# Kernel tuning notes

Hardware: AMD Instinct MI355X
Metric: run time of the kernel (lower is better)

Reference implementation:

```python
import jax, jax.numpy as jnp
import numpy as np

HID = 2048
NH = 16
NKV = 16
HD = HID // NH          # 128
ROPE_BASE = 100000.0
ROPE_SCALE = 4.0
B, L = 2, 2048
NEG = -1e9


def rope(x, offset=0):
    # x: [B, NH, L, HD]; half-split (rotate-half) RoPE with linear scaling
    Lx = x.shape[2]
    D = HD // 2
    pos = (jnp.arange(offset, offset + Lx, dtype=jnp.float32) / ROPE_SCALE)  # [L]
    freq = jnp.exp(-jnp.arange(D, dtype=jnp.float32) * (np.log(ROPE_BASE) / D))  # [D]
    m_theta = pos[:, None] * freq[None, :]          # [L, D]
    cos, sin = jnp.cos(m_theta), jnp.sin(m_theta)
    x1, x2 = x[..., :D], x[..., D:]
    rx1 = x1 * cos - x2 * sin
    rx2 = x1 * sin + x2 * cos
    return jnp.concatenate([rx1, rx2], axis=-1)


def setup_inputs() -> dict:
    key = jax.random.key(0)
    ks = jax.random.split(key, 5)
    x = jax.random.normal(ks[0], (B, L, HID), dtype=jnp.float32)
    # additive causal mask [1,1,L,L]
    mask = jnp.triu(jnp.full((L, L), NEG, dtype=jnp.float32), k=1)[None, None]
    Wq = jax.random.normal(ks[1], (HID, NH * HD), dtype=jnp.float32) * 0.02
    Wk = jax.random.normal(ks[2], (HID, NKV * HD), dtype=jnp.float32) * 0.02
    Wv = jax.random.normal(ks[3], (HID, NKV * HD), dtype=jnp.float32) * 0.02
    Wo = jax.random.normal(ks[4], (NH * HD, HID), dtype=jnp.float32) * 0.02
    return {"x": x, "mask": mask, "Wq": Wq, "Wk": Wk, "Wv": Wv, "Wo": Wo}


def reference(x, mask, Wq, Wk, Wv, Wo):
    b, l, _ = x.shape
    scale = HD ** -0.5
    q = (x @ Wq).reshape(b, l, NH, HD).transpose(0, 2, 1, 3)    # [B,NH,L,HD]
    k = (x @ Wk).reshape(b, l, NKV, HD).transpose(0, 2, 1, 3)
    v = (x @ Wv).reshape(b, l, NKV, HD).transpose(0, 2, 1, 3)
    rep = NH // NKV
    if rep > 1:
        k = jnp.repeat(k, rep, axis=1)
        v = jnp.repeat(v, rep, axis=1)
    q = rope(q)
    k = rope(k)
    scores = scale * jnp.einsum('bhqd,bhkd->bhqk', q, k)        # [B,NH,L,L]
    scores = scores + mask
    attn = jax.nn.softmax(scores, axis=-1)
    out = jnp.einsum('bhqk,bhkd->bhqd', attn, v)                # [B,NH,L,HD]
    out = out.transpose(0, 2, 1, 3).reshape(b, l, NH * HD)
    return out @ Wo
```

## Files before the change

### kernel.cpp

```cpp
#include <hip/hip_runtime.h>
#include <math.h>

#define BB   2
#define LL   2048
#define HIDD 2048
#define NHH  16
#define HDD  128
#define QKVN 6144
#define THR2 11.5416f

typedef unsigned short u16;
typedef float  f32x4 __attribute__((ext_vector_type(4)));
typedef __bf16 bf16x8 __attribute__((ext_vector_type(8)));

static __device__ __forceinline__ float exp2_fast(float x){
  return __builtin_amdgcn_exp2f(x);
}
static __device__ __forceinline__ u16 f2bf(float x){
  unsigned u = __float_as_uint(x);
  return (u16)((u + 0x7fffu + ((u >> 16) & 1u)) >> 16);
}
static __device__ __forceinline__ float bf2f(u16 b){
  return __uint_as_float(((unsigned)b) << 16);
}
static __device__ __forceinline__ void gl_lds16(const void* g, void* l){
  __builtin_amdgcn_global_load_lds(
      (__attribute__((address_space(1))) void*)(void*)g,
      (__attribute__((address_space(3))) void*)l,
      16, 0, 0);
}


__global__ void cvt_f32_bf16_k(const float* __restrict__ src, u16* __restrict__ dst, int n4){
  int i = blockIdx.x * blockDim.x + threadIdx.x;
  if (i >= n4) return;
  float4 v = ((const float4*)src)[i];
  ushort4 o;
  o.x = f2bf(v.x); o.y = f2bf(v.y); o.z = f2bf(v.z); o.w = f2bf(v.w);
  ((ushort4*)dst)[i] = o;
}

__global__ void transpose_cvt_k(const float* __restrict__ src, u16* __restrict__ dst, int R, int C){
  __shared__ float t[32][33];
  int c0 = blockIdx.x * 32, r0 = blockIdx.y * 32;
  int tx = threadIdx.x, ty = threadIdx.y;
  #pragma unroll
  for (int i = 0; i < 32; i += 8) t[ty + i][tx] = src[(size_t)(r0 + ty + i) * C + c0 + tx];
  __syncthreads();
  #pragma unroll
  for (int i = 0; i < 32; i += 8) dst[(size_t)(c0 + ty + i) * R + r0 + tx] = f2bf(t[tx][ty + i]);
}

__global__ void rope_k(u16* __restrict__ qkv){
  int idx = blockIdx.x * blockDim.x + threadIdx.x;
  int d   = idx & 63;
  int h   = (idx >> 6) & 15;
  int row = idx >> 10;
  int l   = row & (LL - 1);
  float fr = __expf(-(float)d * 0.17988946f);
  float th = (float)l * 0.25f * fr;
  float s, c;
  sincosf(th, &s, &c);
  size_t base = (size_t)row * QKVN + h * HDD + d;
  #pragma unroll
  for (int part = 0; part < 2; part++){
    float f = (part == 0) ? 0.12753375f : 1.0f;
    float x1 = bf2f(qkv[base]), x2 = bf2f(qkv[base + 64]);
    qkv[base]      = f2bf((x1 * c - x2 * s) * f);
    qkv[base + 64] = f2bf((x1 * s + x2 * c) * f);
    base += HIDD;
  }
}

__global__ void build_vt_k(const u16* __restrict__ qkv, u16* __restrict__ vt){
  __shared__ u16 t[32][33];
  int bh = blockIdx.z;
  int b = bh >> 4, h = bh & 15;
  const u16* src = qkv + (size_t)b * LL * QKVN + 2 * HIDD + h * HDD;
  u16* dst = vt + (size_t)bh * HDD * LL;
  int d0 = blockIdx.x * 32, l0 = blockIdx.y * 32;
  int tx = threadIdx.x, ty = threadIdx.y;
  #pragma unroll
  for (int i = 0; i < 32; i += 8) t[ty + i][tx] = src[(size_t)(l0 + ty + i) * QKVN + d0 + tx];
  __syncthreads();
  #pragma unroll
  for (int i = 0; i < 32; i += 8) dst[(size_t)(d0 + ty + i) * LL + l0 + tx] = t[tx][ty + i];
}


#define G2_STAGE(kt, bsel) do {                                                           \
  _Pragma("unroll")                                                                       \
  for (int i_ = 0; i_ < 2; i_++){                            \
    int c_ = ((i_ * 8 + wv) * 64) + lane;                                                 \
    int p_ = c_ * 16;                                                                     \
    int r_ = p_ >> 7; int cb_ = (p_ & 127) ^ ((r_ & 7) << 4);                             \
    gl_lds16(A + (size_t)(m0 + r_) * K + (kt) + (cb_ >> 1),                               \
             &AB[bsel][((i_ * 8 + wv) * 64) * 8]);                                        \
  }                                                                                       \
  _Pragma("unroll")                                                                       \
  for (int i_ = 0; i_ < 4; i_++){                            \
    int c_ = ((i_ * 8 + wv) * 64) + lane;                                                 \
    int p_ = c_ * 16;                                                                     \
    int r_ = p_ >> 7; int cb_ = (p_ & 127) ^ ((r_ & 7) << 4);                             \
    gl_lds16(Bt + (size_t)(n0 + r_) * K + (kt) + (cb_ >> 1),                              \
             &AB[bsel][8192 + ((i_ * 8 + wv) * 64) * 8]);                                 \
  }                                                                                       \
} while(0)

template<int OUT_BF16>
__global__ __launch_bounds__(512, 1) void gemm_bt2_k(
    const u16* __restrict__ A, const u16* __restrict__ Bt,
    void* __restrict__ Cout, int M, int N, int K)
{
  __shared__ __align__(16) u16 AB[2][24576];
  const int tid = threadIdx.x, lane = tid & 63, wv = tid >> 6;
  const int wr = wv >> 2, wc = wv & 3;
  const int m0 = blockIdx.y * 128, n0 = blockIdx.x * 256;
  const int rq = lane >> 4, cl = lane & 15;
  const int NT = K >> 6;

  const f32x4 Z = {0.f, 0.f, 0.f, 0.f};
  f32x4 acc[4][4];
  #pragma unroll
  for (int m = 0; m < 4; m++)
    #pragma unroll
    for (int n = 0; n < 4; n++) acc[m][n] = Z;

  G2_STAGE(0, 0);
  G2_STAGE(64, 1);
  asm volatile("s_waitcnt vmcnt(6)");
  __builtin_amdgcn_sched_barrier(0);
  __builtin_amdgcn_s_barrier();

  int cur = 0;
  for (int t = 0; t < NT; t++){
    const char* As_ = (const char*)&AB[cur][0];
    const char* Bs_ = (const char*)&AB[cur][8192];

    #pragma unroll
    for (int ks = 0; ks < 2; ks++){
      const int kb = ks * 64 + rq * 16;
      bf16x8 a[4], b[4];
      #pragma unroll
      for (int m = 0; m < 4; m++){
        int r = wr * 64 + m * 16 + cl;
        a[m] = *(const bf16x8*)(As_ + r * 128 + (kb ^ ((r & 7) << 4)));
      }
      #pragma unroll
      for (int n = 0; n < 4; n++){
        int r = wc * 64 + n * 16 + cl;
        b[n] = *(const bf16x8*)(Bs_ + r * 128 + (kb ^ ((r & 7) << 4)));
      }
      __builtin_amdgcn_s_setprio(1);
      #pragma unroll
      for (int m = 0; m < 4; m++)
        #pragma unroll
        for (int n = 0; n < 4; n++)
          acc[m][n] = __builtin_amdgcn_mfma_f32_16x16x32_bf16(a[m], b[n], acc[m][n], 0, 0, 0);
      __builtin_amdgcn_s_setprio(0);
    }

    __builtin_amdgcn_sched_barrier(0);
    __builtin_amdgcn_s_barrier();

    if (t + 2 < NT){
      G2_STAGE((t + 2) * 64, cur);
      asm volatile("s_waitcnt vmcnt(6)");
    } else {
      asm volatile("s_waitcnt vmcnt(0)");
    }
    __builtin_amdgcn_sched_barrier(0);
    __builtin_amdgcn_s_barrier();
    cur ^= 1;
  }

  #pragma unroll
  for (int m = 0; m < 4; m++){
    int gr0 = m0 + wr * 64 + m * 16 + rq * 4;
    #pragma unroll
    for (int n = 0; n < 4; n++){
      int gc = n0 + wc * 64 + n * 16 + cl;
      #pragma unroll
      for (int rr = 0; rr < 4; rr++){
        if (OUT_BF16) ((u16*)Cout)[(size_t)(gr0 + rr) * N + gc] = f2bf(acc[m][n][rr]);
        else          ((float*)Cout)[(size_t)(gr0 + rr) * N + gc] = acc[m][n][rr];
      }
    }
  }
}


#define STAGE_K(jj, bsel) do {                                                            \
  _Pragma("unroll")                                                                       \
  for (int i_ = 0; i_ < 2; i_++){                                                         \
    int fb_ = (i_ * 8 + wv) * 64;                                                         \
    int p_  = (fb_ + lane) * 16;                                                          \
    int r_ = p_ >> 8; int cb_ = (p_ & 255) ^ ((r_ & 7) << 4);                             \
    gl_lds16(qkv + (size_t)(b * LL + (jj) * 64 + r_) * QKVN + HIDD + h * HDD + (cb_ >> 1),\
             &Kb[bsel][fb_ * 8]);                                                         \
  }                                                                                       \
} while(0)

#define STAGE_V(jj) do {                                                                  \
  _Pragma("unroll")                                                                       \
  for (int i_ = 0; i_ < 2; i_++){                                                         \
    int fb_ = (i_ * 8 + wv) * 64;                                                         \
    int p_  = (fb_ + lane) * 16;                                                          \
    int r_ = p_ >> 7; int cb_ = (p_ & 127) ^ ((r_ & 7) << 4);                             \
    gl_lds16(vt + (size_t)(bh * HDD + r_) * LL + (jj) * 64 + (cb_ >> 1), &Vs[fb_ * 8]);   \
  }                                                                                       \
} while(0)

__global__ __launch_bounds__(512, 1) void attn_k(
    const u16* __restrict__ qkv, const u16* __restrict__ vt,
    u16* __restrict__ aout)
{
  __shared__ __align__(16) u16 Kb[2][64 * 128];
  __shared__ __align__(16) u16 Vs[128 * 64];
  const int tid = threadIdx.x, lane = tid & 63, wv = tid >> 6;
  const int bh = blockIdx.x;
  const int pr = blockIdx.y;
  const int b = bh >> 4, h = bh & 15;
  const int rq = lane >> 4, cl = lane & 15;

  bf16x8 ones;
  #pragma unroll
  for (int i = 0; i < 8; i++) ones[i] = (__bf16)1.0f;
  const f32x4 Z = {0.f, 0.f, 0.f, 0.f};

  int cur = 0;
  STAGE_K(0, 0);

  #pragma unroll
  for (int ph = 0; ph < 2; ph++){
    const int qt = ph ? pr : (15 - pr);
    const int nj = 2 * qt + 2;

    bf16x8 qf[4];
    {
      const u16* qb = qkv + (size_t)(b * LL + qt * 128 + wv * 16 + cl) * QKVN + h * HDD + rq * 8;
      #pragma unroll
      for (int ks = 0; ks < 4; ks++) qf[ks] = *(const bf16x8*)(qb + ks * 32);
    }

    f32x4 acco[8], accl;
    float mst[4];
    #pragma unroll
    for (int n = 0; n < 8; n++) acco[n] = Z;
    accl = Z;
    #pragma unroll
    for (int rr = 0; rr < 4; rr++) mst[rr] = -INFINITY;

    const int wrow_hi = qt * 128 + wv * 16 + 15;

    if (ph == 0) __syncthreads();

    for (int j = 0; j < nj; j++){
      if (j + 1 < nj)      STAGE_K(j + 1, cur ^ 1);
      else if (ph == 0)    STAGE_K(0,     cur ^ 1);
      STAGE_V(j);
      const bool act = (j * 64 <= wrow_hi);

      f32x4 sv[4];
      if (act){
        const char* KsC = (const char*)&Kb[cur][0];
        #pragma unroll
        for (int ct = 0; ct < 4; ct++) sv[ct] = Z;
        #pragma unroll
        for (int ks = 0; ks < 4; ks++){
          const int kb = ks * 64 + rq * 16;
          #pragma unroll
          for (int ct = 0; ct < 4; ct++){
            int r = ct * 16 + cl;
            bf16x8 bfr = *(const bf16x8*)(KsC + r * 256 + (kb ^ ((r & 7) << 4)));
            sv[ct] = __builtin_amdgcn_mfma_f32_16x16x32_bf16(qf[ks], bfr, sv[ct], 0, 0, 0);
          }
        }
      }

      __syncthreads();

      if (act){
        char* pbase = (char*)&Kb[cur][0] + wv * 2048;
        const bool msk = (j >= 2 * qt);

        float p4[4][4], lmx[4];
        #pragma unroll
        for (int rr = 0; rr < 4; rr++) lmx[rr] = -1e30f;
        const int qg = qt * 128 + wv * 16 + rq * 4;
        #pragma unroll
        for (int ct = 0; ct < 4; ct++){
          int col = j * 64 + ct * 16 + cl;
          #pragma unroll
          for (int rr = 0; rr < 4; rr++){
            float v = sv[ct][rr];
            if (msk && col > qg + rr) v = -1e30f;
            p4[ct][rr] = v;
            lmx[rr] = fmaxf(lmx[rr], v);
          }
        }
        float need = -1e30f;
        #pragma unroll
        for (int rr = 0; rr < 4; rr++) need = fmaxf(need, lmx[rr] - mst[rr]);
        if (__any(need > THR2)){
          float mx[4];
          #pragma unroll
          for (int rr = 0; rr < 4; rr++) mx[rr] = lmx[rr];
          #pragma unroll
          for (int off = 1; off < 16; off <<= 1)
            #pragma unroll
            for (int rr = 0; rr < 4; rr++)
              mx[rr] = fmaxf(mx[rr], __shfl_xor(mx[rr], off, 64));
          #pragma unroll
          for (int rr = 0; rr < 4; rr++){
            float mn  = fmaxf(mst[rr], mx[rr]);
            float fsc = exp2_fast(mst[rr] - mn);
            mst[rr] = mn;
            accl[rr] *= fsc;
            #pragma unroll
            for (int n = 0; n < 8; n++) acco[n][rr] *= fsc;
          }
        }
        #pragma unroll
        for (int ct = 0; ct < 4; ct++)
          #pragma unroll
          for (int rr = 0; rr < 4; rr++){
            float e = exp2_fast(p4[ct][rr] - mst[rr]);
            int wr = rq * 4 + rr;
            *(u16*)(pbase + wr * 128 + (((ct * 16 + cl) * 2) ^ ((wr & 7) << 4))) = f2bf(e);
          }

        const char* VsC = (const char*)Vs;
        #pragma unroll
        for (int ks = 0; ks < 2; ks++){
          const int kvb = ks * 64 + rq * 16;
          bf16x8 pa = *(const bf16x8*)(pbase + cl * 128 + (kvb ^ ((cl & 7) << 4)));
          accl = __builtin_amdgcn_mfma_f32_16x16x32_bf16(pa, ones, accl, 0, 0, 0);
          #pragma unroll
          for (int n = 0; n < 8; n++){
            int r = n * 16 + cl;
            bf16x8 bfr = *(const bf16x8*)(VsC + r * 128 + (kvb ^ ((r & 7) << 4)));
            acco[n] = __builtin_amdgcn_mfma_f32_16x16x32_bf16(pa, bfr, acco[n], 0, 0, 0);
          }
        }
      }

      __syncthreads();
      cur ^= 1;
    }

    #pragma unroll
    for (int rr = 0; rr < 4; rr++){
      float inv = 1.0f / accl[rr];
      size_t grow = (size_t)(b * LL + qt * 128 + wv * 16 + rq * 4 + rr);
      #pragma unroll
      for (int n = 0; n < 8; n++)
        aout[grow * HIDD + h * HDD + n * 16 + cl] = f2bf(acco[n][rr] * inv);
    }
  }
}


extern "C" void kernel_launch(void* const* d_in, const int* in_sizes, int n_in,
                              void* d_out, int out_size, void* d_ws, size_t ws_size,
                              hipStream_t stream)
{
  const float* x  = (const float*)d_in[0];
  const float* Wq = (const float*)d_in[2];
  const float* Wk = (const float*)d_in[3];
  const float* Wv = (const float*)d_in[4];
  const float* Wo = (const float*)d_in[5];
  float* out = (float*)d_out;

  if (ws_size < 134217728ull) return;

  char* ws = (char*)d_ws;
  u16* xb   = (u16*)(ws);
  u16* Wt   = (u16*)(ws + 16777216ull);
  u16* Wot  = (u16*)(ws + 41943040ull);
  u16* qkv  = (u16*)(ws + 50331648ull);
  u16* vt   = (u16*)(ws + 100663296ull);
  u16* aout = (u16*)(ws + 117440512ull);

  cvt_f32_bf16_k<<<2097152 / 256, 256, 0, stream>>>(x, xb, 2097152);
  dim3 tb(32, 8);
  transpose_cvt_k<<<dim3(64, 64), tb, 0, stream>>>(Wq, Wt,                   2048, 2048);
  transpose_cvt_k<<<dim3(64, 64), tb, 0, stream>>>(Wk, Wt + 2048 * 2048,     2048, 2048);
  transpose_cvt_k<<<dim3(64, 64), tb, 0, stream>>>(Wv, Wt + 2 * 2048 * 2048, 2048, 2048);
  transpose_cvt_k<<<dim3(64, 64), tb, 0, stream>>>(Wo, Wot,                  2048, 2048);

  gemm_bt2_k<1><<<dim3(6144 / 256, 4096 / 128), 512, 0, stream>>>(xb, Wt, qkv, 4096, 6144, 2048);
  rope_k<<<4194304 / 256, 256, 0, stream>>>(qkv);
  build_vt_k<<<dim3(4, 64, 32), tb, 0, stream>>>(qkv, vt);

  attn_k<<<dim3(32, 8), 512, 0, stream>>>(qkv, vt, aout);

  gemm_bt2_k<0><<<dim3(2048 / 256, 4096 / 128), 512, 0, stream>>>(aout, Wot, out, 4096, 2048, 2048);
}
```

Measured before the change: 279.2 us.

## Triple-buffer GEMM LDS and interleave global prefetch with four MFMA sub-phases

The bf16 GEMM moves from double to triple LDS buffering, so the load for tile t+2 can be issued while tile t is being computed, with no separate barrier-then-load step. Each K-tile is split into four phases of LDS reads plus MFMA, and the A and B global-to-LDS prefetches are spread across those phases with barriers between them. The goal is to overlap global loads with MFMA work and shorten the pipeline stall at the end of each iteration. The cost is 50% more LDS, more barriers per tile, and smaller register fragments per phase, and the changed vmcnt accounting risks mistakes.

```diff
diff --git a/kernel.cpp b/kernel.cpp
--- a/kernel.cpp
+++ b/kernel.cpp
@@ -88,23 +88,25 @@
 }
 
 
-#define G2_STAGE(kt, bsel) do {                                                           \
-  _Pragma("unroll")                                                                       \
-  for (int i_ = 0; i_ < 2; i_++){                            \
-    int c_ = ((i_ * 8 + wv) * 64) + lane;                                                 \
-    int p_ = c_ * 16;                                                                     \
-    int r_ = p_ >> 7; int cb_ = (p_ & 127) ^ ((r_ & 7) << 4);                             \
-    gl_lds16(A + (size_t)(m0 + r_) * K + (kt) + (cb_ >> 1),                               \
-             &AB[bsel][((i_ * 8 + wv) * 64) * 8]);                                        \
-  }                                                                                       \
-  _Pragma("unroll")                                                                       \
-  for (int i_ = 0; i_ < 4; i_++){                            \
-    int c_ = ((i_ * 8 + wv) * 64) + lane;                                                 \
-    int p_ = c_ * 16;                                                                     \
-    int r_ = p_ >> 7; int cb_ = (p_ & 127) ^ ((r_ & 7) << 4);                             \
-    gl_lds16(Bt + (size_t)(n0 + r_) * K + (kt) + (cb_ >> 1),                              \
-             &AB[bsel][8192 + ((i_ * 8 + wv) * 64) * 8]);                                 \
-  }                                                                                       \
+#define G2_STG_A(kt, bsel) do {                                                            \
+  _Pragma("unroll")                                                                        \
+  for (int i_ = 0; i_ < 2; i_++){                                                          \
+    int ci_ = ((i_ * 8 + wv) * 64) + lane;                                                 \
+    int p_ = ci_ * 16; int r_ = p_ >> 7; int cb_ = (p_ & 127) ^ ((r_ & 7) << 4);           \
+    gl_lds16(A + (size_t)(m0 + r_) * K + (kt) + (cb_ >> 1),                                \
+             &AB[bsel][((i_ * 8 + wv) * 64) * 8]);                                         \
+  }                                                                                        \
+} while(0)
+
+#define G2_STG_B(kt, bsel, hh) do {                                                        \
+  _Pragma("unroll")                                                                        \
+  for (int i_ = 0; i_ < 2; i_++){                                                          \
+    int bi_ = (hh) * 2 + i_;                                                               \
+    int ci_ = ((bi_ * 8 + wv) * 64) + lane;                                                \
+    int p_ = ci_ * 16; int r_ = p_ >> 7; int cb_ = (p_ & 127) ^ ((r_ & 7) << 4);           \
+    gl_lds16(Bt + (size_t)(n0 + r_) * K + (kt) + (cb_ >> 1),                               \
+             &AB[bsel][8192 + ((bi_ * 8 + wv) * 64) * 8]);                                 \
+  }                                                                                        \
 } while(0)
 
 template<int OUT_BF16>
@@ -112,7 +114,7 @@
     const u16* __restrict__ A, const u16* __restrict__ Bt,
     void* __restrict__ Cout, int M, int N, int K)
 {
-  __shared__ __align__(16) u16 AB[2][24576];
+  __shared__ __align__(16) u16 AB[3][24576];
   const int tid = threadIdx.x, lane = tid & 63, wv = tid >> 6;
   const int wr = wv >> 2, wc = wv & 3;
   const int m0 = blockIdx.y * 128, n0 = blockIdx.x * 256;
@@ -126,52 +128,107 @@
     #pragma unroll
     for (int n = 0; n < 4; n++) acc[m][n] = Z;
 
-  G2_STAGE(0, 0);
-  G2_STAGE(64, 1);
-  asm volatile("s_waitcnt vmcnt(6)");
+  G2_STG_A(0, 0);  G2_STG_B(0, 0, 0);  G2_STG_B(0, 0, 1);
+  G2_STG_A(64, 1); G2_STG_B(64, 1, 0); G2_STG_B(64, 1, 1);
+  asm volatile("s_waitcnt vmcnt(6)" ::: "memory");
   __builtin_amdgcn_sched_barrier(0);
   __builtin_amdgcn_s_barrier();
 
-  int cur = 0;
   for (int t = 0; t < NT; t++){
+    const int cur = t % 3, nxt = (t + 2) % 3;
+    const bool stg = (t + 2 < NT);
+    const int kt2 = (t + 2) << 6;
     const char* As_ = (const char*)&AB[cur][0];
     const char* Bs_ = (const char*)&AB[cur][8192];
-
-    #pragma unroll
-    for (int ks = 0; ks < 2; ks++){
-      const int kb = ks * 64 + rq * 16;
-      bf16x8 a[4], b[4];
-      #pragma unroll
-      for (int m = 0; m < 4; m++){
-        int r = wr * 64 + m * 16 + cl;
-        a[m] = *(const bf16x8*)(As_ + r * 128 + (kb ^ ((r & 7) << 4)));
-      }
-      #pragma unroll
-      for (int n = 0; n < 4; n++){
-        int r = wc * 64 + n * 16 + cl;
-        b[n] = *(const bf16x8*)(Bs_ + r * 128 + (kb ^ ((r & 7) << 4)));
-      }
+    bf16x8 af[4], bf[2];
+
+    {
+      const int kb = rq * 16;
+      #pragma unroll
+      for (int m = 0; m < 4; m++){ int r = wr * 64 + m * 16 + cl;
+        af[m] = *(const bf16x8*)(As_ + r * 128 + (kb ^ ((r & 7) << 4))); }
+      #pragma unroll
+      for (int n = 0; n < 2; n++){ int r = wc * 64 + n * 16 + cl;
+        bf[n] = *(const bf16x8*)(Bs_ + r * 128 + (kb ^ ((r & 7) << 4))); }
+      if (stg) G2_STG_A(kt2, nxt);
+      __builtin_amdgcn_sched_barrier(0);
+      __builtin_amdgcn_s_barrier();
+      asm volatile("s_waitcnt lgkmcnt(0)" ::: "memory");
+      __builtin_amdgcn_sched_barrier(0);
       __builtin_amdgcn_s_setprio(1);
       #pragma unroll
       for (int m = 0; m < 4; m++)
         #pragma unroll
-        for (int n = 0; n < 4; n++)
-          acc[m][n] = __builtin_amdgcn_mfma_f32_16x16x32_bf16(a[m], b[n], acc[m][n], 0, 0, 0);
+        for (int n = 0; n < 2; n++)
+          acc[m][n] = __builtin_amdgcn_mfma_f32_16x16x32_bf16(af[m], bf[n], acc[m][n], 0, 0, 0);
       __builtin_amdgcn_s_setprio(0);
-    }
-
-    __builtin_amdgcn_sched_barrier(0);
-    __builtin_amdgcn_s_barrier();
-
-    if (t + 2 < NT){
-      G2_STAGE((t + 2) * 64, cur);
-      asm volatile("s_waitcnt vmcnt(6)");
-    } else {
-      asm volatile("s_waitcnt vmcnt(0)");
-    }
-    __builtin_amdgcn_sched_barrier(0);
-    __builtin_amdgcn_s_barrier();
-    cur ^= 1;
+      __builtin_amdgcn_sched_barrier(0);
+      __builtin_amdgcn_s_barrier();
+    }
+    {
+      const int kb = rq * 16;
+      #pragma unroll
+      for (int n = 0; n < 2; n++){ int r = wc * 64 + (n + 2) * 16 + cl;
+        bf[n] = *(const bf16x8*)(Bs_ + r * 128 + (kb ^ ((r & 7) << 4))); }
+      if (stg) G2_STG_B(kt2, nxt, 0);
+      __builtin_amdgcn_sched_barrier(0);
+      __builtin_amdgcn_s_barrier();
+      asm volatile("s_waitcnt lgkmcnt(0)" ::: "memory");
+      __builtin_amdgcn_sched_barrier(0);
+      __builtin_amdgcn_s_setprio(1);
+      #pragma unroll
+      for (int m = 0; m < 4; m++)
+        #pragma unroll
+        for (int n = 0; n < 2; n++)
+          acc[m][n + 2] = __builtin_amdgcn_mfma_f32_16x16x32_bf16(af[m], bf[n], acc[m][n + 2], 0, 0, 0);
+      __builtin_amdgcn_s_setprio(0);
+      __builtin_amdgcn_sched_barrier(0);
+      __builtin_amdgcn_s_barrier();
+    }
+    {
+      const int kb = 64 + rq * 16;
+      #pragma unroll
+      for (int m = 0; m < 4; m++){ int r = wr * 64 + m * 16 + cl;
+        af[m] = *(const bf16x8*)(As_ + r * 128 + (kb ^ ((r & 7) << 4))); }
+      #pragma unroll
+      for (int n = 0; n < 2; n++){ int r = wc * 64 + n * 16 + cl;
+        bf[n] = *(const bf16x8*)(Bs_ + r * 128 + (kb ^ ((r & 7) << 4))); }
+      if (stg) G2_STG_B(kt2, nxt, 1);
+      __builtin_amdgcn_sched_barrier(0);
+      __builtin_amdgcn_s_barrier();
+      asm volatile("s_waitcnt lgkmcnt(0)" ::: "memory");
+      __builtin_amdgcn_sched_barrier(0);
+      __builtin_amdgcn_s_setprio(1);
+      #pragma unroll
+      for (int m = 0; m < 4; m++)
+        #pragma unroll
+        for (int n = 0; n < 2; n++)
+          acc[m][n] = __builtin_amdgcn_mfma_f32_16x16x32_bf16(af[m], bf[n], acc[m][n], 0, 0, 0);
+      __builtin_amdgcn_s_setprio(0);
+      __builtin_amdgcn_sched_barrier(0);
+      __builtin_amdgcn_s_barrier();
+    }
+    {
+      const int kb = 64 + rq * 16;
+      #pragma unroll
+      for (int n = 0; n < 2; n++){ int r = wc * 64 + (n + 2) * 16 + cl;
+        bf[n] = *(const bf16x8*)(Bs_ + r * 128 + (kb ^ ((r & 7) << 4))); }
+      __builtin_amdgcn_sched_barrier(0);
+      __builtin_amdgcn_s_barrier();
+      asm volatile("s_waitcnt lgkmcnt(0)" ::: "memory");
+      __builtin_amdgcn_sched_barrier(0);
+      __builtin_amdgcn_s_setprio(1);
+      #pragma unroll
+      for (int m = 0; m < 4; m++)
+        #pragma unroll
+        for (int n = 0; n < 2; n++)
+          acc[m][n + 2] = __builtin_amdgcn_mfma_f32_16x16x32_bf16(af[m], bf[n], acc[m][n + 2], 0, 0, 0);
+      __builtin_amdgcn_s_setprio(0);
+      __builtin_amdgcn_sched_barrier(0);
+      if (stg) asm volatile("s_waitcnt vmcnt(6)" ::: "memory");
+      else     asm volatile("s_waitcnt vmcnt(0)" ::: "memory");
+      __builtin_amdgcn_s_barrier();
+    }
   }
 
   #pragma unroll
```

Measured after the change: 286.6 us. +2.6%, slower.

## Fuse weight transposes into one vectorized kernel and use simpler 128x128 QKV GEMM

Applied to the files above, without the earlier changes.

Replaces four separate fp32-to-bf16 weight transpose launches with a single kernel that handles all four matrices via blockIdx.z. It uses float4 loads, a 64x64 bf16 shared tile, and wide 16-byte stores. The QKV projection switches from the double-buffered 256x128 GEMM with 512 threads to a new single-buffered 128x128, 256-thread GEMM. That GEMM loads through LDS with a swizzle and uses 16x16x32 bf16 MFMA. The goal is to cut launch overhead and improve transpose bandwidth, but the new GEMM drops the prefetch pipelining the old one had.

```diff
diff --git a/kernel.cpp b/kernel.cpp
--- a/kernel.cpp
+++ b/kernel.cpp
@@ -40,15 +40,39 @@
   ((ushort4*)dst)[i] = o;
 }
 
-__global__ void transpose_cvt_k(const float* __restrict__ src, u16* __restrict__ dst, int R, int C){
-  __shared__ float t[32][33];
-  int c0 = blockIdx.x * 32, r0 = blockIdx.y * 32;
-  int tx = threadIdx.x, ty = threadIdx.y;
-  #pragma unroll
-  for (int i = 0; i < 32; i += 8) t[ty + i][tx] = src[(size_t)(r0 + ty + i) * C + c0 + tx];
+__global__ __launch_bounds__(256) void transpose_cvt4_k(
+    const float* __restrict__ Wq, const float* __restrict__ Wk,
+    const float* __restrict__ Wv, const float* __restrict__ Wo,
+    u16* __restrict__ Wt, u16* __restrict__ Wot)
+{
+  __shared__ u16 t[64][66];
+  const int z = blockIdx.z;
+  const float* src = (z == 0) ? Wq : (z == 1) ? Wk : (z == 2) ? Wv : Wo;
+  u16* dst = (z == 3) ? Wot : (Wt + (size_t)z * 2048 * 2048);
+  const int c0 = blockIdx.x * 64, r0 = blockIdx.y * 64;
+  const int tid = threadIdx.x;
+
+  #pragma unroll
+  for (int i = 0; i < 4; i++){
+    int r  = i * 16 + (tid >> 4);
+    int c4 = (tid & 15) * 4;
+    float4 v = *(const float4*)&src[(size_t)(r0 + r) * 2048 + c0 + c4];
+    t[c4 + 0][r] = f2bf(v.x);
+    t[c4 + 1][r] = f2bf(v.y);
+    t[c4 + 2][r] = f2bf(v.z);
+    t[c4 + 3][r] = f2bf(v.w);
+  }
   __syncthreads();
   #pragma unroll
-  for (int i = 0; i < 32; i += 8) dst[(size_t)(c0 + ty + i) * R + r0 + tx] = f2bf(t[tx][ty + i]);
+  for (int i = 0; i < 2; i++){
+    int c  = i * 32 + (tid >> 3);
+    int rs = (tid & 7) * 8;
+    const unsigned* p = (const unsigned*)&t[c][rs];
+    unsigned w0 = p[0], w1 = p[1], w2 = p[2], w3 = p[3];
+    u16* d = &dst[(size_t)(c0 + c) * 2048 + r0 + rs];
+    ((unsigned*)d)[0] = w0; ((unsigned*)d)[1] = w1;
+    ((unsigned*)d)[2] = w2; ((unsigned*)d)[3] = w3;
+  }
 }
 
 __global__ void rope_k(u16* __restrict__ qkv){
@@ -85,6 +109,75 @@
   __syncthreads();
   #pragma unroll
   for (int i = 0; i < 32; i += 8) dst[(size_t)(d0 + ty + i) * LL + l0 + tx] = t[tx][ty + i];
+}
+
+
+template<int OUT_BF16>
+__global__ __launch_bounds__(256) void gemm_bt_k(
+    const u16* __restrict__ A, const u16* __restrict__ Bt,
+    void* __restrict__ Cout, int M, int N, int K)
+{
+  __shared__ __align__(16) u16 As[128 * 64];
+  __shared__ __align__(16) u16 Bs[128 * 64];
+  const int tid = threadIdx.x, lane = tid & 63, wv = tid >> 6;
+  const int wr = wv >> 1, wc = wv & 1;
+  const int m0 = blockIdx.y * 128, n0 = blockIdx.x * 128;
+  const int rq = lane >> 4, cl = lane & 15;
+
+  const f32x4 Z = {0.f, 0.f, 0.f, 0.f};
+  f32x4 acc[4][4];
+  #pragma unroll
+  for (int m = 0; m < 4; m++)
+    #pragma unroll
+    for (int n = 0; n < 4; n++) acc[m][n] = Z;
+
+  for (int kt = 0; kt < K; kt += 64){
+    #pragma unroll
+    for (int i = 0; i < 4; i++){
+      int fb = (i * 4 + wv) * 64;
+      int p  = (fb + lane) * 16;
+      int r  = p >> 7;
+      int cbs = (p & 127) ^ ((r & 7) << 4);
+      gl_lds16(A  + (size_t)(m0 + r) * K + kt + (cbs >> 1), &As[fb * 8]);
+      gl_lds16(Bt + (size_t)(n0 + r) * K + kt + (cbs >> 1), &Bs[fb * 8]);
+    }
+    __syncthreads();
+    #pragma unroll
+    for (int ks = 0; ks < 2; ks++){
+      const int kb = ks * 64 + rq * 16;
+      bf16x8 a[4], b[4];
+      #pragma unroll
+      for (int m = 0; m < 4; m++){
+        int r = wr * 64 + m * 16 + cl;
+        a[m] = *(const bf16x8*)((const char*)As + r * 128 + (kb ^ ((r & 7) << 4)));
+      }
+      #pragma unroll
+      for (int n = 0; n < 4; n++){
+        int r = wc * 64 + n * 16 + cl;
+        b[n] = *(const bf16x8*)((const char*)Bs + r * 128 + (kb ^ ((r & 7) << 4)));
+      }
+      #pragma unroll
+      for (int m = 0; m < 4; m++)
+        #pragma unroll
+        for (int n = 0; n < 4; n++)
+          acc[m][n] = __builtin_amdgcn_mfma_f32_16x16x32_bf16(a[m], b[n], acc[m][n], 0, 0, 0);
+    }
+    __syncthreads();
+  }
+
+  #pragma unroll
+  for (int m = 0; m < 4; m++){
+    int gr0 = m0 + wr * 64 + m * 16 + rq * 4;
+    #pragma unroll
+    for (int n = 0; n < 4; n++){
+      int gc = n0 + wc * 64 + n * 16 + cl;
+      #pragma unroll
+      for (int rr = 0; rr < 4; rr++){
+        if (OUT_BF16) ((u16*)Cout)[(size_t)(gr0 + rr) * N + gc] = f2bf(acc[m][n][rr]);
+        else          ((float*)Cout)[(size_t)(gr0 + rr) * N + gc] = acc[m][n][rr];
+      }
+    }
+  }
 }
 
 
@@ -383,15 +476,11 @@
   u16* aout = (u16*)(ws + 117440512ull);
 
   cvt_f32_bf16_k<<<2097152 / 256, 256, 0, stream>>>(x, xb, 2097152);
-  dim3 tb(32, 8);
-  transpose_cvt_k<<<dim3(64, 64), tb, 0, stream>>>(Wq, Wt,                   2048, 2048);
-  transpose_cvt_k<<<dim3(64, 64), tb, 0, stream>>>(Wk, Wt + 2048 * 2048,     2048, 2048);
-  transpose_cvt_k<<<dim3(64, 64), tb, 0, stream>>>(Wv, Wt + 2 * 2048 * 2048, 2048, 2048);
-  transpose_cvt_k<<<dim3(64, 64), tb, 0, stream>>>(Wo, Wot,                  2048, 2048);
-
-  gemm_bt2_k<1><<<dim3(6144 / 256, 4096 / 128), 512, 0, stream>>>(xb, Wt, qkv, 4096, 6144, 2048);
+  transpose_cvt4_k<<<dim3(32, 32, 4), 256, 0, stream>>>(Wq, Wk, Wv, Wo, Wt, Wot);
+
+  gemm_bt_k<1><<<dim3(6144 / 128, 4096 / 128), 256, 0, stream>>>(xb, Wt, qkv, 4096, 6144, 2048);
   rope_k<<<4194304 / 256, 256, 0, stream>>>(qkv);
-  build_vt_k<<<dim3(4, 64, 32), tb, 0, stream>>>(qkv, vt);
+  build_vt_k<<<dim3(4, 64, 32), dim3(32, 8), 0, stream>>>(qkv, vt);
 
   attn_k<<<dim3(32, 8), 512, 0, stream>>>(qkv, vt, aout);
 
```

After: 277.3 us. About the same (-0.7%).
